# Kernel optimization log

Hardware: AMD Instinct MI355X
Metric: run time of the kernel (lower is better)

## Reference

```python
import jax, jax.numpy as jnp
import numpy as np
import math

B, T = 2, 2048
DIN, D, DOUT = 2048, 512, 32
NB, H = 2, 8
HD = D // H  # 64, even (RoPE requirement)


def _ln(x, g, b, eps=1e-5):
    m = jnp.mean(x, -1, keepdims=True)
    v = jnp.mean((x - m) ** 2, -1, keepdims=True)
    return (x - m) / jnp.sqrt(v + eps) * g + b


def _rope_tables(L):
    inv = 1.0 / (10000.0 ** (jnp.arange(0, HD, 2, dtype=jnp.float32) / HD))
    t = jnp.arange(L, dtype=jnp.float32)
    fr = t[:, None] * inv[None, :]
    emb = jnp.concatenate([fr, fr], -1)  # [L, HD]
    return jnp.cos(emb), jnp.sin(emb)


def _rot_half(x):
    x1, x2 = x[..., ::2], x[..., 1::2]
    return jnp.stack((-x2, x1), axis=-1).reshape(x.shape)


def _apply_rope(q, k, cos, sin):
    cos, sin = cos[None, None], sin[None, None]
    return q * cos + _rot_half(q) * sin, k * cos + _rot_half(k) * sin


def _heads(t):  # [B,L,D] -> [B,H,L,HD]
    b, L, _ = t.shape
    return t.reshape(b, L, H, HD).transpose(0, 2, 1, 3)


def _block(x, h_a1, h_t1, p1, qW, qb, ksW, ksb, vsW, vsb, kaW, kab, vaW, vab,
           ktW, ktb, vtW, vtb, oW, ob, g, lnG, lnB, fW, fb):
    b, t, _ = x.shape
    h_adp = jnp.concatenate([h_a1[:, None, :], p1[:, None, :]], 1)  # [B,2,D]
    h_tsk = h_t1[:, None, :]                                         # [B,1,D]
    q = _heads(x @ qW + qb)
    ks = _heads(x @ ksW + ksb)
    vs = _heads(x @ vsW + vsb)
    cos, sin = _rope_tables(t)
    q, ks = _apply_rope(q, ks, cos, sin)
    ka = _heads(h_adp @ kaW + kab)
    va = _heads(h_adp @ vaW + vab)
    ca, sa = _rope_tables(2)
    _, ka = _apply_rope(ka, ka, ca, sa)
    kt = _heads(h_tsk @ ktW + ktb)
    vt = _heads(h_tsk @ vtW + vtb)
    ct, st = _rope_tables(1)
    _, kt = _apply_rope(kt, kt, ct, st)
    ratio_g = jnp.tanh(g)
    sc = jnp.concatenate([
        jnp.einsum('bhtd,bhsd->bhts', q, ks),
        jnp.einsum('bhtd,bhsd->bhts', q, ka),
        jnp.einsum('bhtd,bhsd->bhts', q, kt) * ratio_g,
    ], -1) / math.sqrt(HD)
    w = jax.nn.softmax(sc, -1)
    v = jnp.concatenate([vs, va, vt], 2)
    out = jnp.einsum('bhts,bhsd->bhtd', w, v).transpose(0, 2, 1, 3).reshape(b, t, D)
    out = out @ oW + ob
    y = out + x
    return jax.nn.relu(_ln(y, lnG, lnB) @ fW + fb)


def _forward(x, h_a, h_t, p, ln1_g, ln1_b, fc1_W, fc1_b,
             blk_qW, blk_qb, blk_ksW, blk_ksb, blk_vsW, blk_vsb,
             blk_kaW, blk_kab, blk_vaW, blk_vab, blk_ktW, blk_ktb,
             blk_vtW, blk_vtb, blk_oW, blk_ob, blk_g,
             blk_lnG, blk_lnB, blk_fW, blk_fb, ln2_g, ln2_b, fc2_W, fc2_b):
    x = jax.nn.relu(_ln(x, ln1_g, ln1_b) @ fc1_W + fc1_b)
    for i in range(NB):
        idx = i + 1
        x = _block(x, h_a[:, idx], h_t[:, idx], p,
                   blk_qW[i], blk_qb[i], blk_ksW[i], blk_ksb[i],
                   blk_vsW[i], blk_vsb[i], blk_kaW[i], blk_kab[i],
                   blk_vaW[i], blk_vab[i], blk_ktW[i], blk_ktb[i],
                   blk_vtW[i], blk_vtb[i], blk_oW[i], blk_ob[i], blk_g[i],
                   blk_lnG[i], blk_lnB[i], blk_fW[i], blk_fb[i])
    return _ln(x, ln2_g, ln2_b) @ fc2_W + fc2_b


def setup_inputs() -> dict:
    key = jax.random.key(0)
    ks = iter(jax.random.split(key, 64))

    def n(shape, s=0.02):
        return jax.random.normal(next(ks), shape, jnp.float32) * s

    return {
        'x': jax.random.normal(next(ks), (B, T, DIN), jnp.float32),
        'h_a': jax.random.normal(next(ks), (B, NB + 1, D), jnp.float32),
        'h_t': jax.random.normal(next(ks), (B, NB + 1, D), jnp.float32),
        'p': jax.random.normal(next(ks), (B, D), jnp.float32),
        'ln1_g': jnp.ones((DIN,), jnp.float32), 'ln1_b': jnp.zeros((DIN,), jnp.float32),
        'fc1_W': n((DIN, D)), 'fc1_b': jnp.zeros((D,), jnp.float32),
        'blk_qW': n((NB, D, D)), 'blk_qb': jnp.zeros((NB, D), jnp.float32),
        'blk_ksW': n((NB, D, D)), 'blk_ksb': jnp.zeros((NB, D), jnp.float32),
        'blk_vsW': n((NB, D, D)), 'blk_vsb': jnp.zeros((NB, D), jnp.float32),
        'blk_kaW': n((NB, D, D)), 'blk_kab': jnp.zeros((NB, D), jnp.float32),
        'blk_vaW': n((NB, D, D)), 'blk_vab': jnp.zeros((NB, D), jnp.float32),
        'blk_ktW': n((NB, D, D)), 'blk_ktb': jnp.zeros((NB, D), jnp.float32),
        'blk_vtW': n((NB, D, D)), 'blk_vtb': jnp.zeros((NB, D), jnp.float32),
        'blk_oW': n((NB, D, D)), 'blk_ob': jnp.zeros((NB, D), jnp.float32),
        'blk_g': n((NB,), 0.5),
        'blk_lnG': jnp.ones((NB, D), jnp.float32), 'blk_lnB': jnp.zeros((NB, D), jnp.float32),
        'blk_fW': n((NB, D, D)), 'blk_fb': jnp.zeros((NB, D), jnp.float32),
        'ln2_g': jnp.ones((D,), jnp.float32), 'ln2_b': jnp.zeros((D,), jnp.float32),
        'fc2_W': n((D, DOUT)), 'fc2_b': jnp.zeros((DOUT,), jnp.float32),
    }


def reference(x, h_a, h_t, p, ln1_g, ln1_b, fc1_W, fc1_b,
              blk_qW, blk_qb, blk_ksW, blk_ksb, blk_vsW, blk_vsb,
              blk_kaW, blk_kab, blk_vaW, blk_vab, blk_ktW, blk_ktb,
              blk_vtW, blk_vtb, blk_oW, blk_ob, blk_g,
              blk_lnG, blk_lnB, blk_fW, blk_fb, ln2_g, ln2_b, fc2_W, fc2_b):
    return _forward(x, h_a, h_t, p, ln1_g, ln1_b, fc1_W, fc1_b,
                    blk_qW, blk_qb, blk_ksW, blk_ksb, blk_vsW, blk_vsb,
                    blk_kaW, blk_kab, blk_vaW, blk_vab, blk_ktW, blk_ktb,
                    blk_vtW, blk_vtb, blk_oW, blk_ob, blk_g,
                    blk_lnG, blk_lnB, blk_fW, blk_fb, ln2_g, ln2_b, fc2_W, fc2_b)
```

## Files before the change

kernel.cpp:

```cpp
#include <hip/hip_runtime.h>
#include <math.h>

constexpr int kB   = 2;
constexpr int kT   = 2048;
constexpr int kDIN = 2048;
constexpr int kD   = 512;
constexpr int kH   = 8;
constexpr int kHD  = 64;
constexpr int kNB  = 2;
constexpr int kM   = kB * kT;
constexpr int kT2  = 2112;
constexpr int kNT  = 33;

using bf16x8 = __attribute__((ext_vector_type(8))) short;
using f32x4  = __attribute__((ext_vector_type(4))) float;

__device__ inline ushort f2bf(float x) {
    uint u = __float_as_uint(x);
    u = (u + 0x7fffu + ((u >> 16) & 1u)) >> 16;
    return (ushort)u;
}
__device__ inline uint pack2(float a, float b) {
    return (uint)f2bf(a) | ((uint)f2bf(b) << 16);
}

__global__ __launch_bounds__(256) void rope_table_kernel(float* __restrict__ tab) {
    int idx = blockIdx.x * blockDim.x + threadIdx.x;
    if (idx >= kT * 32) return;
    int t = idx >> 5, f = idx & 31;
    double inv = pow(10000.0, -(double)f / 32.0);
    double ang = (double)t * inv;
    tab[idx * 2]     = (float)cos(ang);
    tab[idx * 2 + 1] = (float)sin(ang);
}

__global__ __launch_bounds__(256) void row_stats_kernel(const float* __restrict__ A,
                                                        float* __restrict__ stats, int C) {
    int row = blockIdx.x;
    const float4* A4 = (const float4*)(A + (size_t)row * C);
    int nv = C >> 2;
    float s = 0.f, ss = 0.f;
    for (int i = threadIdx.x; i < nv; i += 256) {
        float4 v = A4[i];
        s  += v.x + v.y + v.z + v.w;
        ss += v.x * v.x + v.y * v.y + v.z * v.z + v.w * v.w;
    }
    #pragma unroll
    for (int o = 32; o > 0; o >>= 1) {
        s  += __shfl_down(s, o, 64);
        ss += __shfl_down(ss, o, 64);
    }
    __shared__ float ls[4], lss[4];
    int wid = threadIdx.x >> 6, lane = threadIdx.x & 63;
    if (lane == 0) { ls[wid] = s; lss[wid] = ss; }
    __syncthreads();
    if (threadIdx.x == 0) {
        float S = ls[0] + ls[1] + ls[2] + ls[3];
        float SS = lss[0] + lss[1] + lss[2] + lss[3];
        float mean = S / C;
        float var  = SS / C - mean * mean;
        stats[row * 2]     = mean;
        stats[row * 2 + 1] = rsqrtf(var + 1e-5f);
    }
}

__device__ inline void tp_tile(const float* __restrict__ src, ushort* __restrict__ dst,
                               int K, int N, int k0, int n0, float (*tile)[65]) {
    int tid = threadIdx.x;
    #pragma unroll
    for (int i = 0; i < 4; ++i) {
        int idx = tid + i * 256;
        int r = idx >> 4, c4 = (idx & 15) << 2;
        float4 v = *(const float4*)(src + (size_t)(k0 + r) * N + n0 + c4);
        tile[r][c4 + 0] = v.x; tile[r][c4 + 1] = v.y;
        tile[r][c4 + 2] = v.z; tile[r][c4 + 3] = v.w;
    }
    __syncthreads();
    int d = tid >> 2, kc = (tid & 3) * 16;
    uint* outp = (uint*)(dst + (size_t)(n0 + d) * K + k0 + kc);
    #pragma unroll
    for (int j = 0; j < 8; ++j)
        outp[j] = pack2(tile[kc + 2 * j][d], tile[kc + 2 * j + 1][d]);
}

__global__ __launch_bounds__(256) void wt_pack_fc1_kernel(
    const float* __restrict__ W, ushort* __restrict__ Wt) {
    __shared__ float tile[64][65];
    tp_tile(W, Wt, kDIN, kD, blockIdx.x * 64, blockIdx.y * 64, tile);
}

__global__ __launch_bounds__(256) void wt_pack_blocks_kernel(
    const float* __restrict__ qW, const float* __restrict__ ksW,
    const float* __restrict__ vsW, const float* __restrict__ oW,
    const float* __restrict__ fW, ushort* __restrict__ Wt) {
    __shared__ float tile[64][65];
    int z = blockIdx.z, wsel = z >> 1, blk = z & 1;
    const float* src;
    switch (wsel) {
        case 0: src = qW; break;
        case 1: src = ksW; break;
        case 2: src = vsW; break;
        case 3: src = oW; break;
        default: src = fW; break;
    }
    src += (size_t)blk * kD * kD;
    ushort* dst = Wt + (size_t)z * kD * kD;
    tp_tile(src, dst, kD, kD, blockIdx.x * 64, blockIdx.y * 64, tile);
}

template <bool LN, bool RELU, bool RES>
__global__ __launch_bounds__(256) void gemm_mfma_kernel(
    const float* __restrict__ A, const ushort* __restrict__ Wt,
    const float* __restrict__ bias, const float* __restrict__ stats,
    const float* __restrict__ lnG, const float* __restrict__ lnB,
    const float* __restrict__ res, float* __restrict__ Cout,
    int K, int N) {
    __shared__ ushort As[64 * 32];
    __shared__ ushort Bs[128 * 32];
    int tid = threadIdx.x;
    int l = tid & 63;
    int l15 = l & 15, lg = l >> 4;
    int w = tid >> 6, wm = w >> 1, wn = w & 1;
    int m0 = blockIdx.y * 64, n0 = blockIdx.x * 128;

    int ar = tid >> 2, aq = tid & 3;
    float mean = 0.f, rstd = 0.f;
    if (LN) { mean = stats[(m0 + ar) * 2]; rstd = stats[(m0 + ar) * 2 + 1]; }
    const float* arow_p = A + (size_t)(m0 + ar) * K + aq * 8;
    ushort* as_w = As + ar * 32 + ((aq ^ ((ar >> 2) & 3)) * 8);

    int br = tid >> 1, bh2 = tid & 1;
    const ushort* brow_p = Wt + (size_t)(n0 + br) * K + bh2 * 16;
    int bsw = (br >> 2) & 3;
    ushort* bs_w0 = Bs + br * 32 + (((bh2 * 2    ) ^ bsw) * 8);
    ushort* bs_w1 = Bs + br * 32 + (((bh2 * 2 + 1) ^ bsw) * 8);

    f32x4 acc[2][4];
    #pragma unroll
    for (int mf = 0; mf < 2; ++mf)
        #pragma unroll
        for (int nf = 0; nf < 4; ++nf) acc[mf][nf] = (f32x4){0.f, 0.f, 0.f, 0.f};

    for (int k0 = 0; k0 < K; k0 += 32) {
        __syncthreads();
        {
            float4 v0 = *(const float4*)(arow_p + k0);
            float4 v1 = *(const float4*)(arow_p + k0 + 4);
            if (LN) {
                float4 g0 = *(const float4*)(lnG + k0 + aq * 8);
                float4 g1 = *(const float4*)(lnG + k0 + aq * 8 + 4);
                float4 b0 = *(const float4*)(lnB + k0 + aq * 8);
                float4 b1 = *(const float4*)(lnB + k0 + aq * 8 + 4);
                v0.x = (v0.x - mean) * rstd * g0.x + b0.x;
                v0.y = (v0.y - mean) * rstd * g0.y + b0.y;
                v0.z = (v0.z - mean) * rstd * g0.z + b0.z;
                v0.w = (v0.w - mean) * rstd * g0.w + b0.w;
                v1.x = (v1.x - mean) * rstd * g1.x + b1.x;
                v1.y = (v1.y - mean) * rstd * g1.y + b1.y;
                v1.z = (v1.z - mean) * rstd * g1.z + b1.z;
                v1.w = (v1.w - mean) * rstd * g1.w + b1.w;
            }
            uint4 o;
            o.x = pack2(v0.x, v0.y); o.y = pack2(v0.z, v0.w);
            o.z = pack2(v1.x, v1.y); o.w = pack2(v1.z, v1.w);
            *(uint4*)as_w = o;
        }
        {
            const uint4* src = (const uint4*)(brow_p + k0);
            *(uint4*)bs_w0 = src[0];
            *(uint4*)bs_w1 = src[1];
        }
        __syncthreads();

        bf16x8 af[2], bf[4];
        #pragma unroll
        for (int mf = 0; mf < 2; ++mf) {
            int row = wm * 32 + mf * 16 + l15;
            af[mf] = *(const bf16x8*)(As + row * 32 + ((lg ^ ((row >> 2) & 3)) * 8));
        }
        #pragma unroll
        for (int nf = 0; nf < 4; ++nf) {
            int row = wn * 64 + nf * 16 + l15;
            bf[nf] = *(const bf16x8*)(Bs + row * 32 + ((lg ^ ((row >> 2) & 3)) * 8));
        }
        #pragma unroll
        for (int mf = 0; mf < 2; ++mf)
            #pragma unroll
            for (int nf = 0; nf < 4; ++nf)
                acc[mf][nf] = __builtin_amdgcn_mfma_f32_16x16x32_bf16(
                    af[mf], bf[nf], acc[mf][nf], 0, 0, 0);
    }

    #pragma unroll
    for (int mf = 0; mf < 2; ++mf) {
        #pragma unroll
        for (int r = 0; r < 4; ++r) {
            int row = m0 + wm * 32 + mf * 16 + lg * 4 + r;
            float* crow = Cout + (size_t)row * N;
            const float* rrow = RES ? (res + (size_t)row * N) : nullptr;
            #pragma unroll
            for (int nf = 0; nf < 4; ++nf) {
                int col = n0 + wn * 64 + nf * 16 + l15;
                float c = acc[mf][nf][r] + bias[col];
                if (RES) c += rrow[col];
                if (RELU) c = fmaxf(c, 0.f);
                crow[col] = c;
            }
        }
    }
}

template <bool LN, bool RELU, bool RES>
__global__ __launch_bounds__(256) void gemm_kernel(
    const float* __restrict__ A, const float* __restrict__ W,
    const float* __restrict__ bias, const float* __restrict__ stats,
    const float* __restrict__ lnG, const float* __restrict__ lnB,
    const float* __restrict__ res, float* __restrict__ Cout,
    int K, int N) {
    __shared__ __align__(16) float As[16][68];
    __shared__ __align__(16) float Bs[16][68];
    int tid = threadIdx.x;
    int bm = blockIdx.y, bn = blockIdx.x;
    int tm = tid >> 4, tn = tid & 15;

    int am   = tid >> 2;
    int ak4  = (tid & 3) << 2;
    int arow = bm * 64 + am;
    float mean = 0.f, rstd = 0.f;
    if (LN) { mean = stats[arow * 2]; rstd = stats[arow * 2 + 1]; }

    int bk   = tid >> 4;
    int bn4  = (tid & 15) << 2;
    int bcol = bn * 64 + bn4;

    float acc[4][4] = {};

    for (int k0 = 0; k0 < K; k0 += 16) {
        float4 a = *(const float4*)(A + (size_t)arow * K + k0 + ak4);
        if (LN) {
            float4 gv = *(const float4*)(lnG + k0 + ak4);
            float4 bv = *(const float4*)(lnB + k0 + ak4);
            a.x = (a.x - mean) * rstd * gv.x + bv.x;
            a.y = (a.y - mean) * rstd * gv.y + bv.y;
            a.z = (a.z - mean) * rstd * gv.z + bv.z;
            a.w = (a.w - mean) * rstd * gv.w + bv.w;
        }
        As[ak4 + 0][am] = a.x;
        As[ak4 + 1][am] = a.y;
        As[ak4 + 2][am] = a.z;
        As[ak4 + 3][am] = a.w;

        float4 b = make_float4(0.f, 0.f, 0.f, 0.f);
        if (bcol < N) b = *(const float4*)(W + (size_t)(k0 + bk) * N + bcol);
        *(float4*)&Bs[bk][bn4] = b;

        __syncthreads();
        #pragma unroll
        for (int kk = 0; kk < 16; ++kk) {
            float4 av = *(const float4*)&As[kk][tm << 2];
            float4 bv = *(const float4*)&Bs[kk][tn << 2];
            acc[0][0] += av.x * bv.x; acc[0][1] += av.x * bv.y; acc[0][2] += av.x * bv.z; acc[0][3] += av.x * bv.w;
            acc[1][0] += av.y * bv.x; acc[1][1] += av.y * bv.y; acc[1][2] += av.y * bv.z; acc[1][3] += av.y * bv.w;
            acc[2][0] += av.z * bv.x; acc[2][1] += av.z * bv.y; acc[2][2] += av.z * bv.z; acc[2][3] += av.z * bv.w;
            acc[3][0] += av.w * bv.x; acc[3][1] += av.w * bv.y; acc[3][2] += av.w * bv.z; acc[3][3] += av.w * bv.w;
        }
        __syncthreads();
    }

    int crow0 = bm * 64 + (tm << 2);
    int ccol0 = bn * 64 + (tn << 2);
    if (ccol0 < N) {
        float4 bs = *(const float4*)(bias + ccol0);
        #pragma unroll
        for (int i = 0; i < 4; ++i) {
            float4 c = make_float4(acc[i][0] + bs.x, acc[i][1] + bs.y,
                                   acc[i][2] + bs.z, acc[i][3] + bs.w);
            if (RES) {
                float4 r = *(const float4*)(res + (size_t)(crow0 + i) * N + ccol0);
                c.x += r.x; c.y += r.y; c.z += r.z; c.w += r.w;
            }
            if (RELU) {
                c.x = fmaxf(c.x, 0.f); c.y = fmaxf(c.y, 0.f);
                c.z = fmaxf(c.z, 0.f); c.w = fmaxf(c.w, 0.f);
            }
            *(float4*)(Cout + (size_t)(crow0 + i) * N + ccol0) = c;
        }
    }
}

__global__ __launch_bounds__(256) void rope_pack_kernel(
    const float* __restrict__ q, const float* __restrict__ k,
    const float* __restrict__ tab,
    ushort* __restrict__ Qb, ushort* __restrict__ Kb) {
    int idx = blockIdx.x * blockDim.x + threadIdx.x;
    if (idx >= kM * (kD / 2)) return;
    int row = idx >> 8;
    int pi  = idx & 255;
    int col = pi << 1;
    int b = row >> 11, t = row & (kT - 1);
    int h = col >> 6, hd = col & 63;
    int dl = col & 63;
    int f0 = (dl < 32) ? dl : dl - 32;
    int f1 = f0 + 1;
    const float* tb = tab + (size_t)t * 64;
    float c0 = tb[f0 * 2], s0 = tb[f0 * 2 + 1];
    float c1 = tb[f1 * 2], s1 = tb[f1 * 2 + 1];
    size_t g = (size_t)row * kD + col;
    float2 qv = *(const float2*)(q + g);
    float2 kv = *(const float2*)(k + g);
    float qx = (qv.x * c0 - qv.y * s0) * 0.125f;
    float qy = (qv.y * c1 + qv.x * s1) * 0.125f;
    float kx = kv.x * c0 - kv.y * s0;
    float ky = kv.y * c1 + kv.x * s1;
    size_t qo = ((size_t)(b * kH + h) * kT  + t) * 64 + hd;
    size_t ko = ((size_t)(b * kH + h) * kT2 + t) * 64 + hd;
    *(uint*)(Qb + qo) = pack2(qx, qy);
    *(uint*)(Kb + ko) = pack2(kx, ky);
}

__global__ __launch_bounds__(256) void vt_pack_kernel(
    const float* __restrict__ v, ushort* __restrict__ Vtb) {
    __shared__ float tile[64][65];
    int t0 = blockIdx.x * 64, h = blockIdx.y, b = blockIdx.z;
    int tid = threadIdx.x;
    #pragma unroll
    for (int i = 0; i < 4; ++i) {
        int idx = tid + i * 256;
        int r = idx >> 4, c4 = (idx & 15) << 2;
        float4 val = *(const float4*)(v + ((size_t)(b * kT + t0 + r)) * kD + h * kHD + c4);
        tile[r][c4 + 0] = val.x; tile[r][c4 + 1] = val.y;
        tile[r][c4 + 2] = val.z; tile[r][c4 + 3] = val.w;
    }
    __syncthreads();
    int d = tid >> 2, tc = (tid & 3) * 16;
    size_t base = ((size_t)(b * kH + h) * kHD + d) * kT2 + t0 + tc;
    uint* outp = (uint*)(Vtb + base);
    #pragma unroll
    for (int j = 0; j < 8; ++j)
        outp[j] = pack2(tile[tc + 2 * j][d], tile[tc + 2 * j + 1][d]);
}

__global__ __launch_bounds__(256) void adapter_kernel(
    const float* __restrict__ h_a, const float* __restrict__ h_t, const float* __restrict__ p,
    const float* __restrict__ kaW, const float* __restrict__ kab,
    const float* __restrict__ vaW, const float* __restrict__ vab,
    const float* __restrict__ ktW, const float* __restrict__ ktb,
    const float* __restrict__ vtW, const float* __restrict__ vtb,
    const float* __restrict__ gscal, const float* __restrict__ tab,
    float* __restrict__ ka, float* __restrict__ va,
    float* __restrict__ kt, float* __restrict__ vt, int blk) {
    __shared__ float in[kD];
    int wg = blockIdx.x;
    int b = wg / 6, which = wg % 6;
    const float* ha_row = h_a + ((size_t)b * (kNB + 1) + blk + 1) * kD;
    const float* ht_row = h_t + ((size_t)b * (kNB + 1) + blk + 1) * kD;
    const float* p_row  = p + (size_t)b * kD;
    const float* inrow; const float* W; const float* bias; float* outrow;
    switch (which) {
        case 0: inrow = ha_row; W = kaW; bias = kab; outrow = ka + (size_t)(b * 2 + 0) * kD; break;
        case 1: inrow = p_row;  W = kaW; bias = kab; outrow = ka + (size_t)(b * 2 + 1) * kD; break;
        case 2: inrow = ha_row; W = vaW; bias = vab; outrow = va + (size_t)(b * 2 + 0) * kD; break;
        case 3: inrow = p_row;  W = vaW; bias = vab; outrow = va + (size_t)(b * 2 + 1) * kD; break;
        case 4: inrow = ht_row; W = ktW; bias = ktb; outrow = kt + (size_t)b * kD; break;
        default: inrow = ht_row; W = vtW; bias = vtb; outrow = vt + (size_t)b * kD; break;
    }
    W += (size_t)blk * kD * kD;
    bias += (size_t)blk * kD;
    int tid = threadIdx.x;
    in[tid * 2]     = inrow[tid * 2];
    in[tid * 2 + 1] = inrow[tid * 2 + 1];
    __syncthreads();
    float a0 = 0.f, a1 = 0.f;
    int c0 = tid * 2;
    for (int kk = 0; kk < kD; ++kk) {
        float x = in[kk];
        float2 w = *(const float2*)(W + (size_t)kk * kD + c0);
        a0 += x * w.x; a1 += x * w.y;
    }
    a0 += bias[c0]; a1 += bias[c0 + 1];
    if (which == 1) {
        int dl = c0 & 63;
        int f0 = (dl < 32) ? dl : dl - 32;
        int f1 = f0 + 1;
        const float* tb = tab + (size_t)1 * 64;
        float cc0 = tb[f0 * 2], ss0 = tb[f0 * 2 + 1];
        float cc1 = tb[f1 * 2], ss1 = tb[f1 * 2 + 1];
        float n0 = a0 * cc0 - a1 * ss0;
        float n1 = a1 * cc1 + a0 * ss1;
        a0 = n0; a1 = n1;
    }
    if (which == 4) {
        float r = tanhf(gscal[blk]);
        a0 *= r; a1 *= r;
    }
    outrow[c0] = a0; outrow[c0 + 1] = a1;
}

__global__ __launch_bounds__(256) void tailpack_kernel(
    const float* __restrict__ ka, const float* __restrict__ va,
    const float* __restrict__ ktp, const float* __restrict__ vtp,
    ushort* __restrict__ Kb, ushort* __restrict__ Vtb) {
    int bh = blockIdx.x; int b = bh >> 3, h = bh & 7;
    int tid = threadIdx.x;
    {
        int row = tid >> 2, dc = (tid & 3) * 16;
        const float* src = nullptr;
        if (row < 2)       src = ka  + (size_t)(b * 2 + row) * kD + h * kHD;
        else if (row == 2) src = ktp + (size_t)b * kD + h * kHD;
        size_t off = ((size_t)(b * kH + h) * kT2 + 2048 + row) * 64 + dc;
        uint* outp = (uint*)(Kb + off);
        #pragma unroll
        for (int j = 0; j < 8; ++j) {
            float a0 = src ? src[dc + 2 * j]     : 0.f;
            float a1 = src ? src[dc + 2 * j + 1] : 0.f;
            outp[j] = pack2(a0, a1);
        }
    }
    {
        int d = tid >> 2, kc = (tid & 3) * 16;
        float v0 = va[(size_t)(b * 2 + 0) * kD + h * kHD + d];
        float v1 = va[(size_t)(b * 2 + 1) * kD + h * kHD + d];
        float v2 = vtp[(size_t)b * kD + h * kHD + d];
        size_t off = ((size_t)(b * kH + h) * kHD + d) * kT2 + 2048 + kc;
        uint* outp = (uint*)(Vtb + off);
        #pragma unroll
        for (int j = 0; j < 8; ++j) {
            int k0 = kc + 2 * j, k1 = k0 + 1;
            float a0 = (k0 == 0) ? v0 : (k0 == 1) ? v1 : (k0 == 2) ? v2 : 0.f;
            float a1 = (k1 == 1) ? v1 : (k1 == 2) ? v2 : 0.f;
            outp[j] = pack2(a0, a1);
        }
    }
}

__global__ __launch_bounds__(256) void attn_mfma_kernel(
    const ushort* __restrict__ Qb, const ushort* __restrict__ Kb,
    const ushort* __restrict__ Vtb, float* __restrict__ out) {
    __shared__ ushort Ks[64 * 64];
    __shared__ ushort Vts[64 * 64];
    __shared__ ushort Ps[4][16 * 64];
    int tid = threadIdx.x;
    int w = tid >> 6, l = tid & 63;
    int l15 = l & 15, lg = l >> 4;
    int h = blockIdx.y, b = blockIdx.z;
    int tq0 = blockIdx.x * 64;
    const size_t bh = (size_t)(b * kH + h);

    const ushort* qptr = Qb + (bh * kT + tq0 + w * 16 + l15) * 64 + lg * 8;
    bf16x8 qf0 = *(const bf16x8*)(qptr);
    bf16x8 qf1 = *(const bf16x8*)(qptr + 32);

    float m_run[4], l_run[4];
    #pragma unroll
    for (int r = 0; r < 4; ++r) { m_run[r] = -1e30f; l_run[r] = 0.f; }
    f32x4 acc[4];
    #pragma unroll
    for (int dt = 0; dt < 4; ++dt) acc[dt] = (f32x4){0.f, 0.f, 0.f, 0.f};

    ushort* Pw = Ps[w];
    const int swzr = (l15 & 7) << 4;

    for (int tile = 0; tile < kNT; ++tile) {
        __syncthreads();
        {
            int r = tid >> 2, c = tid & 3;
            const uint4* src = (const uint4*)(Kb + (bh * kT2 + (size_t)tile * 64 + r) * 64 + c * 16);
            uint4 v0 = src[0], v1 = src[1];
            int sw = (r & 7) << 4;
            char* dst = (char*)Ks + r * 128;
            *(uint4*)(dst + ((c * 32)      ^ sw)) = v0;
            *(uint4*)(dst + ((c * 32 + 16) ^ sw)) = v1;
        }
        {
            int r = tid >> 2, c = tid & 3;
            const uint4* src = (const uint4*)(Vtb + (bh * kHD + r) * kT2 + (size_t)tile * 64 + c * 16);
            uint4 v0 = src[0], v1 = src[1];
            int sw = (r & 7) << 4;
            char* dst = (char*)Vts + r * 128;
            *(uint4*)(dst + ((c * 32)      ^ sw)) = v0;
            *(uint4*)(dst + ((c * 32 + 16) ^ sw)) = v1;
        }
        __syncthreads();

        f32x4 s[4];
        #pragma unroll
        for (int kt = 0; kt < 4; ++kt) {
            const char* krow = (const char*)Ks + (kt * 16 + l15) * 128;
            bf16x8 kf0 = *(const bf16x8*)(krow + ((lg * 16)      ^ swzr));
            bf16x8 kf1 = *(const bf16x8*)(krow + ((64 + lg * 16) ^ swzr));
            f32x4 z = (f32x4){0.f, 0.f, 0.f, 0.f};
            z = __builtin_amdgcn_mfma_f32_16x16x32_bf16(qf0, kf0, z, 0, 0, 0);
            z = __builtin_amdgcn_mfma_f32_16x16x32_bf16(qf1, kf1, z, 0, 0, 0);
            s[kt] = z;
        }
        if (tile == kNT - 1) {
            #pragma unroll
            for (int kt = 0; kt < 4; ++kt) {
                int key = 2048 + kt * 16 + l15;
                if (key >= 2051) {
                    #pragma unroll
                    for (int r = 0; r < 4; ++r) s[kt][r] = -1e30f;
                }
            }
        }

        float mr[4];
        #pragma unroll
        for (int r = 0; r < 4; ++r)
            mr[r] = fmaxf(fmaxf(s[0][r], s[1][r]), fmaxf(s[2][r], s[3][r]));
        #pragma unroll
        for (int mk = 1; mk < 16; mk <<= 1) {
            #pragma unroll
            for (int r = 0; r < 4; ++r) mr[r] = fmaxf(mr[r], __shfl_xor(mr[r], mk, 64));
        }
        float alpha[4], ps[4];
        #pragma unroll
        for (int r = 0; r < 4; ++r) {
            float nm = fmaxf(m_run[r], mr[r]);
            alpha[r] = __expf(m_run[r] - nm);
            m_run[r] = nm;
            ps[r] = 0.f;
        }
        #pragma unroll
        for (int kt = 0; kt < 4; ++kt) {
            #pragma unroll
            for (int r = 0; r < 4; ++r) {
                float pv = __expf(s[kt][r] - m_run[r]);
                s[kt][r] = pv;
                ps[r] += pv;
            }
        }
        #pragma unroll
        for (int mk = 1; mk < 16; mk <<= 1) {
            #pragma unroll
            for (int r = 0; r < 4; ++r) ps[r] += __shfl_xor(ps[r], mk, 64);
        }
        #pragma unroll
        for (int r = 0; r < 4; ++r) l_run[r] = l_run[r] * alpha[r] + ps[r];
        #pragma unroll
        for (int dt = 0; dt < 4; ++dt) {
            #pragma unroll
            for (int r = 0; r < 4; ++r) acc[dt][r] *= alpha[r];
        }

        #pragma unroll
        for (int kt = 0; kt < 4; ++kt) {
            #pragma unroll
            for (int r = 0; r < 4; ++r) {
                int qq = lg * 4 + r;
                int byteoff = qq * 128 + (((kt * 16 + l15) * 2) ^ ((qq & 7) << 4));
                *(ushort*)((char*)Pw + byteoff) = f2bf(s[kt][r]);
            }
        }
        bf16x8 pf0 = *(const bf16x8*)((const char*)Pw + l15 * 128 + ((lg * 16)      ^ swzr));
        bf16x8 pf1 = *(const bf16x8*)((const char*)Pw + l15 * 128 + ((64 + lg * 16) ^ swzr));
        #pragma unroll
        for (int dt = 0; dt < 4; ++dt) {
            const char* vrow = (const char*)Vts + (dt * 16 + l15) * 128;
            bf16x8 vf0 = *(const bf16x8*)(vrow + ((lg * 16)      ^ swzr));
            bf16x8 vf1 = *(const bf16x8*)(vrow + ((64 + lg * 16) ^ swzr));
            acc[dt] = __builtin_amdgcn_mfma_f32_16x16x32_bf16(pf0, vf0, acc[dt], 0, 0, 0);
            acc[dt] = __builtin_amdgcn_mfma_f32_16x16x32_bf16(pf1, vf1, acc[dt], 0, 0, 0);
        }
    }

    #pragma unroll
    for (int r = 0; r < 4; ++r) {
        float inv = 1.f / l_run[r];
        int t = tq0 + w * 16 + lg * 4 + r;
        float* orow = out + ((size_t)(b * kT + t)) * kD + h * kHD;
        #pragma unroll
        for (int dt = 0; dt < 4; ++dt)
            orow[dt * 16 + l15] = acc[dt][r] * inv;
    }
}

extern "C" void kernel_launch(void* const* d_in, const int* in_sizes, int n_in,
                              void* d_out, int out_size, void* d_ws, size_t ws_size,
                              hipStream_t stream) {
    const float* x      = (const float*)d_in[0];
    const float* h_a    = (const float*)d_in[1];
    const float* h_t    = (const float*)d_in[2];
    const float* p      = (const float*)d_in[3];
    const float* ln1_g  = (const float*)d_in[4];
    const float* ln1_b  = (const float*)d_in[5];
    const float* fc1_W  = (const float*)d_in[6];
    const float* fc1_b  = (const float*)d_in[7];
    const float* blk_qW  = (const float*)d_in[8];
    const float* blk_qb  = (const float*)d_in[9];
    const float* blk_ksW = (const float*)d_in[10];
    const float* blk_ksb = (const float*)d_in[11];
    const float* blk_vsW = (const float*)d_in[12];
    const float* blk_vsb = (const float*)d_in[13];
    const float* blk_kaW = (const float*)d_in[14];
    const float* blk_kab = (const float*)d_in[15];
    const float* blk_vaW = (const float*)d_in[16];
    const float* blk_vab = (const float*)d_in[17];
    const float* blk_ktW = (const float*)d_in[18];
    const float* blk_ktb = (const float*)d_in[19];
    const float* blk_vtW = (const float*)d_in[20];
    const float* blk_vtb = (const float*)d_in[21];
    const float* blk_oW  = (const float*)d_in[22];
    const float* blk_ob  = (const float*)d_in[23];
    const float* blk_g   = (const float*)d_in[24];
    const float* blk_lnG = (const float*)d_in[25];
    const float* blk_lnB = (const float*)d_in[26];
    const float* blk_fW  = (const float*)d_in[27];
    const float* blk_fb  = (const float*)d_in[28];
    const float* ln2_g  = (const float*)d_in[29];
    const float* ln2_b  = (const float*)d_in[30];
    const float* fc2_W  = (const float*)d_in[31];
    const float* fc2_b  = (const float*)d_in[32];
    float* out = (float*)d_out;

    float* ws = (float*)d_ws;
    size_t o = 0;
    float* rope_tab = ws + o; o += (size_t)kT * 32 * 2;
    float* stats    = ws + o; o += (size_t)kM * 2;
    float* bufX     = ws + o; o += (size_t)kM * kD;
    float* bufQ     = ws + o; o += (size_t)kM * kD;
    float* bufK     = ws + o; o += (size_t)kM * kD;
    float* bufV     = ws + o; o += (size_t)kM * kD;
    float* ka_buf   = ws + o; o += (size_t)kB * 2 * kD;
    float* va_buf   = ws + o; o += (size_t)kB * 2 * kD;
    float* kt_buf   = ws + o; o += (size_t)kB * kD;
    float* vt_buf   = ws + o; o += (size_t)kB * kD;
    ushort* Qb  = (ushort*)(ws + o); o += (size_t)kB * kH * kT  * kHD / 2;
    ushort* Kb  = (ushort*)(ws + o); o += (size_t)kB * kH * kT2 * kHD / 2;
    ushort* Vtb = (ushort*)(ws + o); o += (size_t)kB * kH * kT2 * kHD / 2;
    ushort* Wt_fc1 = (ushort*)(ws + o); o += (size_t)kD * kDIN / 2;
    ushort* Wt_blk = (ushort*)(ws + o); o += (size_t)10 * kD * kD / 2;

    dim3 blk256(256);
    dim3 mf_grid(kD / 128, kM / 64);
    dim3 fc2_grid(1, kM / 64);
    dim3 attn_grid(kT / 64, kH, kB);
    dim3 vtp_grid(kT / 64, kH, kB);
    dim3 tp_fc1_grid(kDIN / 64, kD / 64);
    dim3 tp_blk_grid(kD / 64, kD / 64, 10);

    rope_table_kernel<<<(kT * 32 + 255) / 256, blk256, 0, stream>>>(rope_tab);

    wt_pack_fc1_kernel<<<tp_fc1_grid, blk256, 0, stream>>>(fc1_W, Wt_fc1);
    wt_pack_blocks_kernel<<<tp_blk_grid, blk256, 0, stream>>>(
        blk_qW, blk_ksW, blk_vsW, blk_oW, blk_fW, Wt_blk);

    row_stats_kernel<<<kM, blk256, 0, stream>>>(x, stats, kDIN);
    gemm_mfma_kernel<true, true, false><<<mf_grid, blk256, 0, stream>>>(
        x, Wt_fc1, fc1_b, stats, ln1_g, ln1_b, nullptr, bufX, kDIN, kD);

    for (int blk = 0; blk < kNB; ++blk) {
        const size_t wsz = (size_t)kD * kD;
        const ushort* qWt  = Wt_blk + (0 * 2 + blk) * wsz;
        const ushort* ksWt = Wt_blk + (1 * 2 + blk) * wsz;
        const ushort* vsWt = Wt_blk + (2 * 2 + blk) * wsz;
        const ushort* oWt  = Wt_blk + (3 * 2 + blk) * wsz;
        const ushort* fWt  = Wt_blk + (4 * 2 + blk) * wsz;
        const float* qb  = blk_qb  + (size_t)blk * kD;
        const float* ksb = blk_ksb + (size_t)blk * kD;
        const float* vsb = blk_vsb + (size_t)blk * kD;
        const float* ob  = blk_ob  + (size_t)blk * kD;
        const float* fb  = blk_fb  + (size_t)blk * kD;
        const float* lnG = blk_lnG + (size_t)blk * kD;
        const float* lnB = blk_lnB + (size_t)blk * kD;

        gemm_mfma_kernel<false, false, false><<<mf_grid, blk256, 0, stream>>>(
            bufX, qWt, qb, nullptr, nullptr, nullptr, nullptr, bufQ, kD, kD);
        gemm_mfma_kernel<false, false, false><<<mf_grid, blk256, 0, stream>>>(
            bufX, ksWt, ksb, nullptr, nullptr, nullptr, nullptr, bufK, kD, kD);
        gemm_mfma_kernel<false, false, false><<<mf_grid, blk256, 0, stream>>>(
            bufX, vsWt, vsb, nullptr, nullptr, nullptr, nullptr, bufV, kD, kD);

        rope_pack_kernel<<<kM, blk256, 0, stream>>>(bufQ, bufK, rope_tab, Qb, Kb);
        vt_pack_kernel<<<vtp_grid, blk256, 0, stream>>>(bufV, Vtb);

        adapter_kernel<<<12, blk256, 0, stream>>>(
            h_a, h_t, p, blk_kaW, blk_kab, blk_vaW, blk_vab,
            blk_ktW, blk_ktb, blk_vtW, blk_vtb, blk_g, rope_tab,
            ka_buf, va_buf, kt_buf, vt_buf, blk);
        tailpack_kernel<<<16, blk256, 0, stream>>>(
            ka_buf, va_buf, kt_buf, vt_buf, Kb, Vtb);

        attn_mfma_kernel<<<attn_grid, blk256, 0, stream>>>(Qb, Kb, Vtb, bufQ);

        gemm_mfma_kernel<false, false, true><<<mf_grid, blk256, 0, stream>>>(
            bufQ, oWt, ob, nullptr, nullptr, nullptr, bufX, bufV, kD, kD);

        row_stats_kernel<<<kM, blk256, 0, stream>>>(bufV, stats, kD);
        gemm_mfma_kernel<true, true, false><<<mf_grid, blk256, 0, stream>>>(
            bufV, fWt, fb, stats, lnG, lnB, nullptr, bufX, kD, kD);
    }

    row_stats_kernel<<<kM, blk256, 0, stream>>>(bufX, stats, kD);
    gemm_kernel<true, false, false><<<fc2_grid, blk256, 0, stream>>>(
        bufX, fc2_W, fc2_b, stats, ln2_g, ln2_b, nullptr, out, kD, 32);
}
```

Measured before the change: 624.3 us.

## Use bf16 GEMM inputs, 64x64x64 tiles, and register-prefetch K/V tiles in attention

```diff
diff --git a/kernel.cpp b/kernel.cpp
--- a/kernel.cpp
+++ b/kernel.cpp
@@ -108,87 +108,98 @@
     tp_tile(src, dst, kD, kD, blockIdx.x * 64, blockIdx.y * 64, tile);
 }
 
-template <bool LN, bool RELU, bool RES>
-__global__ __launch_bounds__(256) void gemm_mfma_kernel(
-    const float* __restrict__ A, const ushort* __restrict__ Wt,
-    const float* __restrict__ bias, const float* __restrict__ stats,
-    const float* __restrict__ lnG, const float* __restrict__ lnB,
-    const float* __restrict__ res, float* __restrict__ Cout,
-    int K, int N) {
-    __shared__ ushort As[64 * 32];
-    __shared__ ushort Bs[128 * 32];
+template <int AMODE, bool RELU, bool RES, bool DUAL>
+__global__ __launch_bounds__(256) void gemm_bf16_kernel(
+    const float* __restrict__ Af, const ushort* __restrict__ Ab,
+    const ushort* __restrict__ Wt, const float* __restrict__ bias,
+    const float* __restrict__ stats, const float* __restrict__ lnG,
+    const float* __restrict__ lnB, const float* __restrict__ res,
+    float* __restrict__ Cout, ushort* __restrict__ Cb, int K, int N) {
+    __shared__ ushort As[64 * 64];
+    __shared__ ushort Bs[64 * 64];
     int tid = threadIdx.x;
-    int l = tid & 63;
-    int l15 = l & 15, lg = l >> 4;
+    int l15 = tid & 15, lg = (tid >> 4) & 3;
     int w = tid >> 6, wm = w >> 1, wn = w & 1;
-    int m0 = blockIdx.y * 64, n0 = blockIdx.x * 128;
+    int m0 = blockIdx.y * 64, n0 = blockIdx.x * 64;
 
     int ar = tid >> 2, aq = tid & 3;
     float mean = 0.f, rstd = 0.f;
-    if (LN) { mean = stats[(m0 + ar) * 2]; rstd = stats[(m0 + ar) * 2 + 1]; }
-    const float* arow_p = A + (size_t)(m0 + ar) * K + aq * 8;
-    ushort* as_w = As + ar * 32 + ((aq ^ ((ar >> 2) & 3)) * 8);
-
-    int br = tid >> 1, bh2 = tid & 1;
-    const ushort* brow_p = Wt + (size_t)(n0 + br) * K + bh2 * 16;
-    int bsw = (br >> 2) & 3;
-    ushort* bs_w0 = Bs + br * 32 + (((bh2 * 2    ) ^ bsw) * 8);
-    ushort* bs_w1 = Bs + br * 32 + (((bh2 * 2 + 1) ^ bsw) * 8);
-
-    f32x4 acc[2][4];
+    if (AMODE == 2) { mean = stats[(m0 + ar) * 2]; rstd = stats[(m0 + ar) * 2 + 1]; }
+    ushort* as_w0 = As + ar * 64 + (( aq      ^ (ar & 7)) * 8);
+    ushort* as_w1 = As + ar * 64 + (((aq + 4) ^ (ar & 7)) * 8);
+    ushort* bs_w0 = Bs + ar * 64 + (( aq      ^ (ar & 7)) * 8);
+    ushort* bs_w1 = Bs + ar * 64 + (((aq + 4) ^ (ar & 7)) * 8);
+    const ushort* brow = Wt + (size_t)(n0 + ar) * K;
+
+    f32x4 acc[2][2];
     #pragma unroll
     for (int mf = 0; mf < 2; ++mf)
         #pragma unroll
-        for (int nf = 0; nf < 4; ++nf) acc[mf][nf] = (f32x4){0.f, 0.f, 0.f, 0.f};
-
-    for (int k0 = 0; k0 < K; k0 += 32) {
+        for (int nf = 0; nf < 2; ++nf) acc[mf][nf] = (f32x4){0.f, 0.f, 0.f, 0.f};
+
+    for (int k0 = 0; k0 < K; k0 += 64) {
         __syncthreads();
+        if (AMODE == 0) {
+            const uint4* s = (const uint4*)(Ab + (size_t)(m0 + ar) * K + k0) + aq;
+            *(uint4*)as_w0 = s[0];
+            *(uint4*)as_w1 = s[4];
+        } else {
+            const float* ap = Af + (size_t)(m0 + ar) * K + k0 + aq * 8;
+            float4 v0 = *(const float4*)(ap);
+            float4 v1 = *(const float4*)(ap + 4);
+            float4 v2 = *(const float4*)(ap + 32);
+            float4 v3 = *(const float4*)(ap + 36);
+            if (AMODE == 2) {
+                const float* gp = lnG + k0 + aq * 8;
+                const float* bp = lnB + k0 + aq * 8;
+                float4 g0 = *(const float4*)(gp),      g1 = *(const float4*)(gp + 4);
+                float4 g2 = *(const float4*)(gp + 32), g3 = *(const float4*)(gp + 36);
+                float4 b0 = *(const float4*)(bp),      b1 = *(const float4*)(bp + 4);
+                float4 b2 = *(const float4*)(bp + 32), b3 = *(const float4*)(bp + 36);
+                v0.x = (v0.x - mean) * rstd * g0.x + b0.x; v0.y = (v0.y - mean) * rstd * g0.y + b0.y;
+                v0.z = (v0.z - mean) * rstd * g0.z + b0.z; v0.w = (v0.w - mean) * rstd * g0.w + b0.w;
+                v1.x = (v1.x - mean) * rstd * g1.x + b1.x; v1.y = (v1.y - mean) * rstd * g1.y + b1.y;
+                v1.z = (v1.z - mean) * rstd * g1.z + b1.z; v1.w = (v1.w - mean) * rstd * g1.w + b1.w;
+                v2.x = (v2.x - mean) * rstd * g2.x + b2.x; v2.y = (v2.y - mean) * rstd * g2.y + b2.y;
+                v2.z = (v2.z - mean) * rstd * g2.z + b2.z; v2.w = (v2.w - mean) * rstd * g2.w + b2.w;
+                v3.x = (v3.x - mean) * rstd * g3.x + b3.x; v3.y = (v3.y - mean) * rstd * g3.y + b3.y;
+                v3.z = (v3.z - mean) * rstd * g3.z + b3.z; v3.w = (v3.w - mean) * rstd * g3.w + b3.w;
+            }
+            uint4 o0, o1;
+            o0.x = pack2(v0.x, v0.y); o0.y = pack2(v0.z, v0.w);
+            o0.z = pack2(v1.x, v1.y); o0.w = pack2(v1.z, v1.w);
+            o1.x = pack2(v2.x, v2.y); o1.y = pack2(v2.z, v2.w);
+            o1.z = pack2(v3.x, v3.y); o1.w = pack2(v3.z, v3.w);
+            *(uint4*)as_w0 = o0;
+            *(uint4*)as_w1 = o1;
+        }
         {
-            float4 v0 = *(const float4*)(arow_p + k0);
-            float4 v1 = *(const float4*)(arow_p + k0 + 4);
-            if (LN) {
-                float4 g0 = *(const float4*)(lnG + k0 + aq * 8);
-                float4 g1 = *(const float4*)(lnG + k0 + aq * 8 + 4);
-                float4 b0 = *(const float4*)(lnB + k0 + aq * 8);
-                float4 b1 = *(const float4*)(lnB + k0 + aq * 8 + 4);
-                v0.x = (v0.x - mean) * rstd * g0.x + b0.x;
-                v0.y = (v0.y - mean) * rstd * g0.y + b0.y;
-                v0.z = (v0.z - mean) * rstd * g0.z + b0.z;
-                v0.w = (v0.w - mean) * rstd * g0.w + b0.w;
-                v1.x = (v1.x - mean) * rstd * g1.x + b1.x;
-                v1.y = (v1.y - mean) * rstd * g1.y + b1.y;
-                v1.z = (v1.z - mean) * rstd * g1.z + b1.z;
-                v1.w = (v1.w - mean) * rstd * g1.w + b1.w;
-            }
-            uint4 o;
-            o.x = pack2(v0.x, v0.y); o.y = pack2(v0.z, v0.w);
-            o.z = pack2(v1.x, v1.y); o.w = pack2(v1.z, v1.w);
-            *(uint4*)as_w = o;
-        }
-        {
-            const uint4* src = (const uint4*)(brow_p + k0);
-            *(uint4*)bs_w0 = src[0];
-            *(uint4*)bs_w1 = src[1];
+            const uint4* s = (const uint4*)(brow + k0) + aq;
+            *(uint4*)bs_w0 = s[0];
+            *(uint4*)bs_w1 = s[4];
         }
         __syncthreads();
 
-        bf16x8 af[2], bf[4];
-        #pragma unroll
-        for (int mf = 0; mf < 2; ++mf) {
-            int row = wm * 32 + mf * 16 + l15;
-            af[mf] = *(const bf16x8*)(As + row * 32 + ((lg ^ ((row >> 2) & 3)) * 8));
-        }
-        #pragma unroll
-        for (int nf = 0; nf < 4; ++nf) {
-            int row = wn * 64 + nf * 16 + l15;
-            bf[nf] = *(const bf16x8*)(Bs + row * 32 + ((lg ^ ((row >> 2) & 3)) * 8));
-        }
-        #pragma unroll
-        for (int mf = 0; mf < 2; ++mf)
-            #pragma unroll
-            for (int nf = 0; nf < 4; ++nf)
-                acc[mf][nf] = __builtin_amdgcn_mfma_f32_16x16x32_bf16(
-                    af[mf], bf[nf], acc[mf][nf], 0, 0, 0);
+        #pragma unroll
+        for (int kk = 0; kk < 2; ++kk) {
+            bf16x8 af[2], bfr[2];
+            #pragma unroll
+            for (int mf = 0; mf < 2; ++mf) {
+                int row = wm * 32 + mf * 16 + l15;
+                af[mf] = *(const bf16x8*)(As + row * 64 + (((kk * 4 + lg) ^ (row & 7)) * 8));
+            }
+            #pragma unroll
+            for (int nf = 0; nf < 2; ++nf) {
+                int row = wn * 32 + nf * 16 + l15;
+                bfr[nf] = *(const bf16x8*)(Bs + row * 64 + (((kk * 4 + lg) ^ (row & 7)) * 8));
+            }
+            #pragma unroll
+            for (int mf = 0; mf < 2; ++mf)
+                #pragma unroll
+                for (int nf = 0; nf < 2; ++nf)
+                    acc[mf][nf] = __builtin_amdgcn_mfma_f32_16x16x32_bf16(
+                        af[mf], bfr[nf], acc[mf][nf], 0, 0, 0);
+        }
     }
 
     #pragma unroll
@@ -197,14 +208,16 @@
         for (int r = 0; r < 4; ++r) {
             int row = m0 + wm * 32 + mf * 16 + lg * 4 + r;
             float* crow = Cout + (size_t)row * N;
+            ushort* cbrow = DUAL ? (Cb + (size_t)row * N) : nullptr;
             const float* rrow = RES ? (res + (size_t)row * N) : nullptr;
             #pragma unroll
-            for (int nf = 0; nf < 4; ++nf) {
-                int col = n0 + wn * 64 + nf * 16 + l15;
+            for (int nf = 0; nf < 2; ++nf) {
+                int col = n0 + wn * 32 + nf * 16 + l15;
                 float c = acc[mf][nf][r] + bias[col];
                 if (RES) c += rrow[col];
                 if (RELU) c = fmaxf(c, 0.f);
                 crow[col] = c;
+                if (DUAL) cbrow[col] = f2bf(c);
             }
         }
     }
@@ -435,7 +448,7 @@
 
 __global__ __launch_bounds__(256) void attn_mfma_kernel(
     const ushort* __restrict__ Qb, const ushort* __restrict__ Kb,
-    const ushort* __restrict__ Vtb, float* __restrict__ out) {
+    const ushort* __restrict__ Vtb, ushort* __restrict__ AOb) {
     __shared__ ushort Ks[64 * 64];
     __shared__ ushort Vts[64 * 64];
     __shared__ ushort Ps[4][16 * 64];
@@ -460,27 +473,33 @@
     ushort* Pw = Ps[w];
     const int swzr = (l15 & 7) << 4;
 
+    int sr = tid >> 2, sc = tid & 3;
+    const int sw = (sr & 7) << 4;
+    uint4 kra, krb, vra, vrb;
+    {
+        const uint4* ks = (const uint4*)(Kb + (bh * kT2 + sr) * 64 + sc * 16);
+        kra = ks[0]; krb = ks[1];
+        const uint4* vs = (const uint4*)(Vtb + (bh * kHD + sr) * kT2 + sc * 16);
+        vra = vs[0]; vrb = vs[1];
+    }
+
     for (int tile = 0; tile < kNT; ++tile) {
         __syncthreads();
         {
-            int r = tid >> 2, c = tid & 3;
-            const uint4* src = (const uint4*)(Kb + (bh * kT2 + (size_t)tile * 64 + r) * 64 + c * 16);
-            uint4 v0 = src[0], v1 = src[1];
-            int sw = (r & 7) << 4;
-            char* dst = (char*)Ks + r * 128;
-            *(uint4*)(dst + ((c * 32)      ^ sw)) = v0;
-            *(uint4*)(dst + ((c * 32 + 16) ^ sw)) = v1;
-        }
-        {
-            int r = tid >> 2, c = tid & 3;
-            const uint4* src = (const uint4*)(Vtb + (bh * kHD + r) * kT2 + (size_t)tile * 64 + c * 16);
-            uint4 v0 = src[0], v1 = src[1];
-            int sw = (r & 7) << 4;
-            char* dst = (char*)Vts + r * 128;
-            *(uint4*)(dst + ((c * 32)      ^ sw)) = v0;
-            *(uint4*)(dst + ((c * 32 + 16) ^ sw)) = v1;
+            char* dk = (char*)Ks + sr * 128;
+            *(uint4*)(dk + ((sc * 32)      ^ sw)) = kra;
+            *(uint4*)(dk + ((sc * 32 + 16) ^ sw)) = krb;
+            char* dv = (char*)Vts + sr * 128;
+            *(uint4*)(dv + ((sc * 32)      ^ sw)) = vra;
+            *(uint4*)(dv + ((sc * 32 + 16) ^ sw)) = vrb;
         }
         __syncthreads();
+        if (tile + 1 < kNT) {
+            const uint4* ks = (const uint4*)(Kb + (bh * kT2 + (size_t)(tile + 1) * 64 + sr) * 64 + sc * 16);
+            kra = ks[0]; krb = ks[1];
+            const uint4* vs = (const uint4*)(Vtb + (bh * kHD + sr) * kT2 + (size_t)(tile + 1) * 64 + sc * 16);
+            vra = vs[0]; vrb = vs[1];
+        }
 
         f32x4 s[4];
         #pragma unroll
@@ -568,10 +587,10 @@
     for (int r = 0; r < 4; ++r) {
         float inv = 1.f / l_run[r];
         int t = tq0 + w * 16 + lg * 4 + r;
-        float* orow = out + ((size_t)(b * kT + t)) * kD + h * kHD;
+        ushort* orow = AOb + ((size_t)(b * kT + t)) * kD + h * kHD;
         #pragma unroll
         for (int dt = 0; dt < 4; ++dt)
-            orow[dt * 16 + l15] = acc[dt][r] * inv;
+            orow[dt * 16 + l15] = f2bf(acc[dt][r] * inv);
     }
 }
 
@@ -625,14 +644,16 @@
     float* va_buf   = ws + o; o += (size_t)kB * 2 * kD;
     float* kt_buf   = ws + o; o += (size_t)kB * kD;
     float* vt_buf   = ws + o; o += (size_t)kB * kD;
-    ushort* Qb  = (ushort*)(ws + o); o += (size_t)kB * kH * kT  * kHD / 2;
-    ushort* Kb  = (ushort*)(ws + o); o += (size_t)kB * kH * kT2 * kHD / 2;
-    ushort* Vtb = (ushort*)(ws + o); o += (size_t)kB * kH * kT2 * kHD / 2;
+    ushort* Qb   = (ushort*)(ws + o); o += (size_t)kB * kH * kT  * kHD / 2;
+    ushort* Kb   = (ushort*)(ws + o); o += (size_t)kB * kH * kT2 * kHD / 2;
+    ushort* Vtb  = (ushort*)(ws + o); o += (size_t)kB * kH * kT2 * kHD / 2;
     ushort* Wt_fc1 = (ushort*)(ws + o); o += (size_t)kD * kDIN / 2;
     ushort* Wt_blk = (ushort*)(ws + o); o += (size_t)10 * kD * kD / 2;
+    ushort* bufXb  = (ushort*)(ws + o); o += (size_t)kM * kD / 2;
+    ushort* AOb    = (ushort*)(ws + o); o += (size_t)kM * kD / 2;
 
     dim3 blk256(256);
-    dim3 mf_grid(kD / 128, kM / 64);
+    dim3 mf_grid(kD / 64, kM / 64);
     dim3 fc2_grid(1, kM / 64);
     dim3 attn_grid(kT / 64, kH, kB);
     dim3 vtp_grid(kT / 64, kH, kB);
@@ -646,8 +667,9 @@
         blk_qW, blk_ksW, blk_vsW, blk_oW, blk_fW, Wt_blk);
 
     row_stats_kernel<<<kM, blk256, 0, stream>>>(x, stats, kDIN);
-    gemm_mfma_kernel<true, true, false><<<mf_grid, blk256, 0, stream>>>(
-        x, Wt_fc1, fc1_b, stats, ln1_g, ln1_b, nullptr, bufX, kDIN, kD);
+    gemm_bf16_kernel<2, true, false, true><<<mf_grid, blk256, 0, stream>>>(
+        x, nullptr, Wt_fc1, fc1_b, stats, ln1_g, ln1_b, nullptr,
+        bufX, bufXb, kDIN, kD);
 
     for (int blk = 0; blk < kNB; ++blk) {
         const size_t wsz = (size_t)kD * kD;
@@ -664,12 +686,15 @@
         const float* lnG = blk_lnG + (size_t)blk * kD;
         const float* lnB = blk_lnB + (size_t)blk * kD;
 
-        gemm_mfma_kernel<false, false, false><<<mf_grid, blk256, 0, stream>>>(
-            bufX, qWt, qb, nullptr, nullptr, nullptr, nullptr, bufQ, kD, kD);
-        gemm_mfma_kernel<false, false, false><<<mf_grid, blk256, 0, stream>>>(
-            bufX, ksWt, ksb, nullptr, nullptr, nullptr, nullptr, bufK, kD, kD);
-        gemm_mfma_kernel<false, false, false><<<mf_grid, blk256, 0, stream>>>(
-            bufX, vsWt, vsb, nullptr, nullptr, nullptr, nullptr, bufV, kD, kD);
+        gemm_bf16_kernel<0, false, false, false><<<mf_grid, blk256, 0, stream>>>(
+            nullptr, bufXb, qWt, qb, nullptr, nullptr, nullptr, nullptr,
+            bufQ, nullptr, kD, kD);
+        gemm_bf16_kernel<0, false, false, false><<<mf_grid, blk256, 0, stream>>>(
+            nullptr, bufXb, ksWt, ksb, nullptr, nullptr, nullptr, nullptr,
+            bufK, nullptr, kD, kD);
+        gemm_bf16_kernel<0, false, false, false><<<mf_grid, blk256, 0, stream>>>(
+            nullptr, bufXb, vsWt, vsb, nullptr, nullptr, nullptr, nullptr,
+            bufV, nullptr, kD, kD);
 
         rope_pack_kernel<<<kM, blk256, 0, stream>>>(bufQ, bufK, rope_tab, Qb, Kb);
         vt_pack_kernel<<<vtp_grid, blk256, 0, stream>>>(bufV, Vtb);
@@ -681,14 +706,16 @@
         tailpack_kernel<<<16, blk256, 0, stream>>>(
             ka_buf, va_buf, kt_buf, vt_buf, Kb, Vtb);
 
-        attn_mfma_kernel<<<attn_grid, blk256, 0, stream>>>(Qb, Kb, Vtb, bufQ);
-
-        gemm_mfma_kernel<false, false, true><<<mf_grid, blk256, 0, stream>>>(
-            bufQ, oWt, ob, nullptr, nullptr, nullptr, bufX, bufV, kD, kD);
+        attn_mfma_kernel<<<attn_grid, blk256, 0, stream>>>(Qb, Kb, Vtb, AOb);
+
+        gemm_bf16_kernel<0, false, true, false><<<mf_grid, blk256, 0, stream>>>(
+            nullptr, AOb, oWt, ob, nullptr, nullptr, nullptr, bufX,
+            bufV, nullptr, kD, kD);
 
         row_stats_kernel<<<kM, blk256, 0, stream>>>(bufV, stats, kD);
-        gemm_mfma_kernel<true, true, false><<<mf_grid, blk256, 0, stream>>>(
-            bufV, fWt, fb, stats, lnG, lnB, nullptr, bufX, kD, kD);
+        gemm_bf16_kernel<2, true, false, true><<<mf_grid, blk256, 0, stream>>>(
+            bufV, nullptr, fWt, fb, stats, lnG, lnB, nullptr,
+            bufX, bufXb, kD, kD);
     }
 
     row_stats_kernel<<<kM, blk256, 0, stream>>>(bufX, stats, kD);
```

New measurement: 572.2 us. -8.3%, faster.
